# Optimization experiments

Hardware: AMD Instinct MI355X
Metric: run time of the kernel (lower is better)

Reference implementation:

```python
import jax, jax.numpy as jnp
import numpy as np

V, E, H, O, S, N = 32000, 256, 512, 32000, 128, 256

def setup_inputs() -> dict:
    key = jax.random.key(0)
    ks = jax.random.split(key, 12)
    s = 0.05
    return {
        'x': jax.random.randint(ks[0], (N, 1), 0, V),
        'encoder_outputs': jax.random.normal(ks[1], (N, S, 2 * H), jnp.float32),
        'hidden': jax.random.normal(ks[2], (1, N, H), jnp.float32),
        'cell': jax.random.normal(ks[3], (1, N, H), jnp.float32),
        'emb': jax.random.normal(ks[4], (V, E), jnp.float32) * s,
        'W_energy': jax.random.normal(ks[5], (1, 3 * H), jnp.float32) * s,
        'b_energy': jnp.zeros((1,), jnp.float32),
        'W_ih': jax.random.normal(ks[6], (4 * H, E + 2 * H), jnp.float32) * s,
        'W_hh': jax.random.normal(ks[7], (4 * H, H), jnp.float32) * s,
        'b_ih': jnp.zeros((4 * H,), jnp.float32),
        'b_hh': jnp.zeros((4 * H,), jnp.float32),
        'W_out': jax.random.normal(ks[8], (O, H), jnp.float32) * s,
        'b_out': jnp.zeros((O,), jnp.float32),
    }

def reference(x, encoder_outputs, hidden, cell, emb, W_energy, b_energy,
              W_ih, W_hh, b_ih, b_hh, W_out, b_out):
    # Dropout is identity at inference (eval mode).
    embedding = emb[x]                      # [N,1,E]
    n, s, _ = encoder_outputs.shape
    h = hidden[0]                            # [N,H] (num_layers==1)
    h_rep = jnp.broadcast_to(h[:, None, :], (n, s, h.shape[-1]))  # [N,S,H]
    feat = jnp.concatenate([h_rep, encoder_outputs], axis=-1)     # [N,S,3H]
    energy = jax.nn.relu(feat @ W_energy.T + b_energy)            # [N,S,1]
    attention = jax.nn.softmax(energy, axis=1)                    # softmax over seq
    context = jnp.einsum('nsk,nsl->nkl', attention, encoder_outputs)  # [N,1,2H]
    lstm_in = jnp.concatenate([context, embedding], axis=-1)[:, 0, :]  # [N,E+2H]
    gates = lstm_in @ W_ih.T + b_ih + h @ W_hh.T + b_hh           # [N,4H]
    i, f, g, o = jnp.split(gates, 4, axis=-1)                     # torch gate order
    i, f, o = jax.nn.sigmoid(i), jax.nn.sigmoid(f), jax.nn.sigmoid(o)
    g = jnp.tanh(g)
    c_new = f * cell[0] + i * g
    h_new = o * jnp.tanh(c_new)
    outputs = h_new[:, None, :]                                   # [N,1,H]
    predictions = outputs @ W_out.T + b_out                       # [N,1,O]
    return predictions, h_new[None], c_new[None]
```

## Files before the change

### kernel.cpp

```cpp
#include <hip/hip_runtime.h>
#include <hip/hip_bf16.h>

#define N_ 256
#define S_ 128
#define H_ 512
#define E_ 256
#define O_ 32000
#define KZ 1792
#define GJ 2048
#define KSPLIT 4
#define KCHUNK 448

typedef __attribute__((ext_vector_type(8))) short sv8;
typedef __attribute__((ext_vector_type(4))) float fv4;

__device__ __forceinline__ unsigned short f2bf(float f) {
  return __builtin_bit_cast(unsigned short, __float2bfloat16(f));
}

__device__ __forceinline__ sv8 pack8(fv4 a, fv4 b) {
  sv8 r;
  r[0] = (short)f2bf(a[0]); r[1] = (short)f2bf(a[1]);
  r[2] = (short)f2bf(a[2]); r[3] = (short)f2bf(a[3]);
  r[4] = (short)f2bf(b[0]); r[5] = (short)f2bf(b[1]);
  r[6] = (short)f2bf(b[2]); r[7] = (short)f2bf(b[3]);
  return r;
}

__global__ __launch_bounds__(1024) void k_attn(
    const int* __restrict__ x, const float* __restrict__ eo,
    const float* __restrict__ hid, const float* __restrict__ emb,
    const float* __restrict__ We, const float* __restrict__ be,
    const float* __restrict__ Wih, const float* __restrict__ Whh,
    unsigned short* __restrict__ Wgbf, unsigned short* __restrict__ z)
{
  if (blockIdx.y == 1) {
    const int tid = blockIdx.x * 1024 + threadIdx.x;
    for (int g = tid; g < 2048 * 224; g += 256 * 1024) {
      const int j = g / 224, c = g - j * 224;
      sv8* dst = (sv8*)(Wgbf + (size_t)j * KZ);
      if (c < 160) {
        const fv4* src = (const fv4*)(Wih + (size_t)j * 1280);
        dst[c] = pack8(src[2 * c], src[2 * c + 1]);
      } else {
        const int cc = c - 160;
        const fv4* src = (const fv4*)(Whh + (size_t)j * 512);
        dst[c] = pack8(src[2 * cc], src[2 * cc + 1]);
      }
    }
    return;
  }

  const int n = blockIdx.x;
  const int t = threadIdx.x;
  const int w = t >> 6;
  const int l = t & 63;

  __shared__ float s_red[16];
  __shared__ float s_m[16], s_l[16];
  __shared__ float s_ctx[16][1024];

  float hv = (t < 512) ? hid[(size_t)n * H_ + t] * We[t] : 0.f;
  #pragma unroll
  for (int off = 32; off >= 1; off >>= 1) hv += __shfl_xor(hv, off);
  if (l == 0) s_red[w] = hv;
  __syncthreads();
  float hWe = be[0];
  #pragma unroll
  for (int i = 0; i < 8; ++i) hWe += s_red[i];

  fv4 we0, we1, we2, we3;
  {
    const fv4* wp = (const fv4*)(We + H_);
    we0 = wp[l]; we1 = wp[l + 64]; we2 = wp[l + 128]; we3 = wp[l + 192];
  }

  float m = 0.f, lsum = 0.f;
  fv4 c0 = {0,0,0,0}, c1 = {0,0,0,0}, c2 = {0,0,0,0}, c3 = {0,0,0,0};
  const float* eob = eo + ((size_t)n * S_ + w * 8) * 1024;
  #pragma unroll 2
  for (int i = 0; i < 8; ++i) {
    const fv4* p = (const fv4*)(eob + (size_t)i * 1024);
    fv4 v0 = p[l], v1 = p[l + 64], v2 = p[l + 128], v3 = p[l + 192];
    float d = 0.f;
    #pragma unroll
    for (int c = 0; c < 4; ++c)
      d += v0[c]*we0[c] + v1[c]*we1[c] + v2[c]*we2[c] + v3[c]*we3[c];
    #pragma unroll
    for (int off = 32; off >= 1; off >>= 1) d += __shfl_xor(d, off);
    const float e  = fmaxf(d + hWe, 0.f);
    const float mn = fmaxf(m, e);
    const float sc = __expf(m - mn);
    const float pp = __expf(e - mn);
    lsum = lsum * sc + pp;
    #pragma unroll
    for (int c = 0; c < 4; ++c) {
      c0[c] = c0[c]*sc + pp*v0[c];
      c1[c] = c1[c]*sc + pp*v1[c];
      c2[c] = c2[c]*sc + pp*v2[c];
      c3[c] = c3[c]*sc + pp*v3[c];
    }
    m = mn;
  }
  if (l == 0) { s_m[w] = m; s_l[w] = lsum; }
  {
    fv4* sc_ = (fv4*)s_ctx[w];
    sc_[l] = c0; sc_[l+64] = c1; sc_[l+128] = c2; sc_[l+192] = c3;
  }
  __syncthreads();

  float M = s_m[0];
  #pragma unroll
  for (int i = 1; i < 16; ++i) M = fmaxf(M, s_m[i]);
  float wgt[16]; float L = 0.f;
  #pragma unroll
  for (int i = 0; i < 16; ++i) { wgt[i] = __expf(s_m[i] - M); L += wgt[i] * s_l[i]; }
  const float rL = 1.f / L;

  float acc = 0.f;
  #pragma unroll
  for (int i = 0; i < 16; ++i) acc += wgt[i] * s_ctx[i][t];
  unsigned short* zr = z + (size_t)n * KZ;
  zr[t] = f2bf(acc * rL);

  if (t < 256)       zr[1024 + t] = f2bf(emb[(size_t)x[n] * E_ + t]);
  else if (t < 768)  zr[1024 + t] = f2bf(hid[(size_t)n * H_ + (t - 256)]);
}

__global__ __launch_bounds__(256) void k_gates(
    const unsigned short* __restrict__ z, const unsigned short* __restrict__ Wgbf,
    float* __restrict__ part)
{
  const int j0 = blockIdx.x * 64;
  const int n0 = blockIdx.y * 64;
  const int kc = blockIdx.z * KCHUNK;
  const int t = threadIdx.x;
  const int w = t >> 6, l = t & 63;
  const int lr = l & 15, lg = l >> 4;
  const int jb = j0 + w * 16 + lr;

  const unsigned short* arow = z + kc + 8 * lg;
  const unsigned short* wrow = Wgbf + (size_t)jb * KZ + kc + 8 * lg;

  fv4 acc[4] = {{0,0,0,0},{0,0,0,0},{0,0,0,0},{0,0,0,0}};
  #pragma unroll
  for (int s = 0; s < 14; ++s) {
    const sv8 bf = *(const sv8*)(wrow + s * 32);
    #pragma unroll
    for (int f = 0; f < 4; ++f) {
      const sv8 af = *(const sv8*)(arow + (size_t)(n0 + f*16 + lr) * KZ + s * 32);
      acc[f] = __builtin_amdgcn_mfma_f32_16x16x32_bf16(af, bf, acc[f], 0, 0, 0);
    }
  }
  float* pp = part + (size_t)blockIdx.z * (N_ * GJ);
  #pragma unroll
  for (int f = 0; f < 4; ++f) {
    #pragma unroll
    for (int r = 0; r < 4; ++r)
      pp[(size_t)(n0 + f*16 + lg*4 + r) * GJ + jb] = acc[f][r];
  }
}

__global__ __launch_bounds__(256) void k_lstm(
    const float* __restrict__ part, const float* __restrict__ cell,
    const float* __restrict__ bih, const float* __restrict__ bhh,
    float* __restrict__ hout, float* __restrict__ cout,
    unsigned short* __restrict__ hbf)
{
  const int tid = blockIdx.x * 256 + threadIdx.x;
  const int n = tid >> 9, hh = tid & 511;
  const size_t base = (size_t)n * GJ;
  float ig = bih[hh]        + bhh[hh];
  float fg = bih[512 + hh]  + bhh[512 + hh];
  float gg = bih[1024 + hh] + bhh[1024 + hh];
  float og = bih[1536 + hh] + bhh[1536 + hh];
  #pragma unroll
  for (int k = 0; k < KSPLIT; ++k) {
    const float* p = part + (size_t)k * (N_ * GJ) + base;
    ig += p[hh];
    fg += p[512 + hh];
    gg += p[1024 + hh];
    og += p[1536 + hh];
  }
  ig = 1.f / (1.f + __expf(-ig));
  fg = 1.f / (1.f + __expf(-fg));
  og = 1.f / (1.f + __expf(-og));
  gg = tanhf(gg);
  const float c = fg * cell[tid] + ig * gg;
  const float h = og * tanhf(c);
  cout[tid] = c;
  hout[tid] = h;
  hbf[tid] = f2bf(h);
}

__global__ __launch_bounds__(512, 2) void k_pred(
    const unsigned short* __restrict__ hbf, const float* __restrict__ Wout,
    const float* __restrict__ bout, float* __restrict__ pred)
{
  __shared__ unsigned short Blds[64 * 512];
  const int o0 = blockIdx.x * 64;
  const int t = threadIdx.x;

  #pragma unroll
  for (int i = 0; i < 8; ++i) {
    const int g = t + i * 512;
    const int row = g >> 6, c = g & 63;
    const fv4* src = (const fv4*)(Wout + (size_t)(o0 + row) * H_ + c * 8);
    const sv8 v = pack8(src[0], src[1]);
    *(sv8*)((char*)Blds + row * 1024 + ((c * 16) ^ ((row & 7) << 4))) = v;
  }
  __syncthreads();

  const int w = t >> 6, l = t & 63;
  const int lr = l & 15, lg = l >> 4;
  const int nr = w * 32;

  fv4 acc[2][4] = {};
  #pragma unroll
  for (int kk = 0; kk < 16; ++kk) {
    sv8 a[2];
    #pragma unroll
    for (int f = 0; f < 2; ++f)
      a[f] = *(const sv8*)(hbf + (size_t)(nr + f*16 + lr) * H_ + kk*32 + 8*lg);
    #pragma unroll
    for (int fo = 0; fo < 4; ++fo) {
      const int row = fo * 16 + lr;
      const sv8 b = *(const sv8*)((const char*)Blds + row * 1024 +
                                  ((kk*64 + lg*16) ^ ((row & 7) << 4)));
      #pragma unroll
      for (int f = 0; f < 2; ++f)
        acc[f][fo] = __builtin_amdgcn_mfma_f32_16x16x32_bf16(b, a[f], acc[f][fo], 0, 0, 0);
    }
  }
  #pragma unroll
  for (int fo = 0; fo < 4; ++fo) {
    const int ob = o0 + fo * 16 + lg * 4;
    const fv4 bo4 = *(const fv4*)(bout + ob);
    #pragma unroll
    for (int f = 0; f < 2; ++f) {
      const int n = nr + f * 16 + lr;
      fv4 v;
      #pragma unroll
      for (int r = 0; r < 4; ++r) v[r] = acc[f][fo][r] + bo4[r];
      *(fv4*)(pred + (size_t)n * O_ + ob) = v;
    }
  }
}

extern "C" void kernel_launch(void* const* d_in, const int* in_sizes, int n_in,
                              void* d_out, int out_size, void* d_ws, size_t ws_size,
                              hipStream_t stream) {
  const int*   x    = (const int*)  d_in[0];
  const float* eo   = (const float*)d_in[1];
  const float* hid  = (const float*)d_in[2];
  const float* cell = (const float*)d_in[3];
  const float* emb  = (const float*)d_in[4];
  const float* We   = (const float*)d_in[5];
  const float* be   = (const float*)d_in[6];
  const float* Wih  = (const float*)d_in[7];
  const float* Whh  = (const float*)d_in[8];
  const float* bih  = (const float*)d_in[9];
  const float* bhh  = (const float*)d_in[10];
  const float* Wout = (const float*)d_in[11];
  const float* bout = (const float*)d_in[12];

  float* pred = (float*)d_out;
  float* hout = pred + (size_t)N_ * O_;
  float* cout = hout + (size_t)N_ * H_;

  unsigned short* z    = (unsigned short*)d_ws;
  unsigned short* hbf  = z + (size_t)N_ * KZ;
  float* part = (float*)(hbf + (size_t)N_ * H_);
  unsigned short* Wgbf = (unsigned short*)(part + (size_t)KSPLIT * N_ * GJ);

  k_attn <<<dim3(256, 2), 1024, 0, stream>>>(x, eo, hid, emb, We, be,
                                             Wih, Whh, Wgbf, z);
  k_gates<<<dim3(32, 4, KSPLIT), 256, 0, stream>>>(z, Wgbf, part);
  k_lstm <<<512, 256, 0, stream>>>(part, cell, bih, bhh, hout, cout, hbf);
  k_pred <<<500, 512, 0, stream>>>(hbf, Wout, bout, pred);
}
```

Baseline: 84.31 us.

## Fuse gates GEMM and LSTM cell into one kernel with grid barrier

Merges the split-K gate GEMM and the LSTM pointwise kernel into a single 512-block launch, separated by a software grid-wide barrier built on global atomics. The barrier counter is reset inside the attention kernel. This removes one kernel launch and its inter-kernel gap. In exchange it relies on all 512 blocks being co-resident, adds spin-wait overhead, and risks deadlock if the blocks cannot all be scheduled at once.

```diff
diff --git a/kernel.cpp b/kernel.cpp
--- a/kernel.cpp
+++ b/kernel.cpp
@@ -32,9 +32,11 @@
     const float* __restrict__ hid, const float* __restrict__ emb,
     const float* __restrict__ We, const float* __restrict__ be,
     const float* __restrict__ Wih, const float* __restrict__ Whh,
-    unsigned short* __restrict__ Wgbf, unsigned short* __restrict__ z)
+    unsigned short* __restrict__ Wgbf, unsigned short* __restrict__ z,
+    int* __restrict__ bar)
 {
   if (blockIdx.y == 1) {
+    if (blockIdx.x == 0 && threadIdx.x == 0) { bar[0] = 0; bar[1] = 0; }
     const int tid = blockIdx.x * 1024 + threadIdx.x;
     for (int g = tid; g < 2048 * 224; g += 256 * 1024) {
       const int j = g / 224, c = g - j * 224;
@@ -127,70 +129,89 @@
   else if (t < 768)  zr[1024 + t] = f2bf(hid[(size_t)n * H_ + (t - 256)]);
 }
 
-__global__ __launch_bounds__(256) void k_gates(
+__global__ __launch_bounds__(256) void k_gl(
     const unsigned short* __restrict__ z, const unsigned short* __restrict__ Wgbf,
-    float* __restrict__ part)
+    float* __restrict__ part, const float* __restrict__ cell,
+    const float* __restrict__ bih, const float* __restrict__ bhh,
+    float* __restrict__ hout, float* __restrict__ cout,
+    unsigned short* __restrict__ hbf, int* __restrict__ bar)
 {
-  const int j0 = blockIdx.x * 64;
-  const int n0 = blockIdx.y * 64;
-  const int kc = blockIdx.z * KCHUNK;
+  const int b = blockIdx.x;
   const int t = threadIdx.x;
   const int w = t >> 6, l = t & 63;
   const int lr = l & 15, lg = l >> 4;
-  const int jb = j0 + w * 16 + lr;
-
-  const unsigned short* arow = z + kc + 8 * lg;
-  const unsigned short* wrow = Wgbf + (size_t)jb * KZ + kc + 8 * lg;
-
-  fv4 acc[4] = {{0,0,0,0},{0,0,0,0},{0,0,0,0},{0,0,0,0}};
-  #pragma unroll
-  for (int s = 0; s < 14; ++s) {
-    const sv8 bf = *(const sv8*)(wrow + s * 32);
+
+  {
+    const int j0   = (b & 31) * 64;
+    const int n0   = ((b >> 5) & 3) * 64;
+    const int kidx = b >> 7;
+    const int kc   = kidx * KCHUNK;
+    const int jb   = j0 + w * 16 + lr;
+
+    const unsigned short* arow = z + kc + 8 * lg;
+    const unsigned short* wrow = Wgbf + (size_t)jb * KZ + kc + 8 * lg;
+
+    fv4 acc[4] = {{0,0,0,0},{0,0,0,0},{0,0,0,0},{0,0,0,0}};
+    #pragma unroll
+    for (int s = 0; s < 14; ++s) {
+      const sv8 bf = *(const sv8*)(wrow + s * 32);
+      #pragma unroll
+      for (int f = 0; f < 4; ++f) {
+        const sv8 af = *(const sv8*)(arow + (size_t)(n0 + f*16 + lr) * KZ + s * 32);
+        acc[f] = __builtin_amdgcn_mfma_f32_16x16x32_bf16(af, bf, acc[f], 0, 0, 0);
+      }
+    }
+    float* pp = part + (size_t)kidx * (N_ * GJ);
     #pragma unroll
     for (int f = 0; f < 4; ++f) {
-      const sv8 af = *(const sv8*)(arow + (size_t)(n0 + f*16 + lr) * KZ + s * 32);
-      acc[f] = __builtin_amdgcn_mfma_f32_16x16x32_bf16(af, bf, acc[f], 0, 0, 0);
-    }
-  }
-  float* pp = part + (size_t)blockIdx.z * (N_ * GJ);
-  #pragma unroll
-  for (int f = 0; f < 4; ++f) {
-    #pragma unroll
-    for (int r = 0; r < 4; ++r)
-      pp[(size_t)(n0 + f*16 + lg*4 + r) * GJ + jb] = acc[f][r];
-  }
-}
-
-__global__ __launch_bounds__(256) void k_lstm(
-    const float* __restrict__ part, const float* __restrict__ cell,
-    const float* __restrict__ bih, const float* __restrict__ bhh,
-    float* __restrict__ hout, float* __restrict__ cout,
-    unsigned short* __restrict__ hbf)
-{
-  const int tid = blockIdx.x * 256 + threadIdx.x;
-  const int n = tid >> 9, hh = tid & 511;
-  const size_t base = (size_t)n * GJ;
-  float ig = bih[hh]        + bhh[hh];
-  float fg = bih[512 + hh]  + bhh[512 + hh];
-  float gg = bih[1024 + hh] + bhh[1024 + hh];
-  float og = bih[1536 + hh] + bhh[1536 + hh];
-  #pragma unroll
-  for (int k = 0; k < KSPLIT; ++k) {
-    const float* p = part + (size_t)k * (N_ * GJ) + base;
-    ig += p[hh];
-    fg += p[512 + hh];
-    gg += p[1024 + hh];
-    og += p[1536 + hh];
-  }
-  ig = 1.f / (1.f + __expf(-ig));
-  fg = 1.f / (1.f + __expf(-fg));
-  og = 1.f / (1.f + __expf(-og));
-  gg = tanhf(gg);
-  const float c = fg * cell[tid] + ig * gg;
-  const float h = og * tanhf(c);
-  cout[tid] = c;
-  hout[tid] = h;
-  hbf[tid] = f2bf(h);
+      #pragma unroll
+      for (int r = 0; r < 4; ++r)
+        pp[(size_t)(n0 + f*16 + lg*4 + r) * GJ + jb] = acc[f][r];
+    }
+  }
+
+  __syncthreads();
+  __threadfence();
+  if (t == 0) {
+    const int g0 = __hip_atomic_load(&bar[1], __ATOMIC_ACQUIRE,
+                                     __HIP_MEMORY_SCOPE_AGENT);
+    if (atomicAdd(&bar[0], 1) == 511) {
+      __hip_atomic_store(&bar[0], 0, __ATOMIC_RELAXED, __HIP_MEMORY_SCOPE_AGENT);
+      __hip_atomic_store(&bar[1], g0 + 1, __ATOMIC_RELEASE,
+                         __HIP_MEMORY_SCOPE_AGENT);
+    } else {
+      while (__hip_atomic_load(&bar[1], __ATOMIC_ACQUIRE,
+                               __HIP_MEMORY_SCOPE_AGENT) == g0) {}
+    }
+  }
+  __syncthreads();
+
+  {
+    const int tid = b * 256 + t;
+    const int n = tid >> 9, hh = tid & 511;
+    const size_t base = (size_t)n * GJ;
+    float ig = bih[hh]        + bhh[hh];
+    float fg = bih[512 + hh]  + bhh[512 + hh];
+    float gg = bih[1024 + hh] + bhh[1024 + hh];
+    float og = bih[1536 + hh] + bhh[1536 + hh];
+    #pragma unroll
+    for (int k = 0; k < KSPLIT; ++k) {
+      const float* p = part + (size_t)k * (N_ * GJ) + base;
+      ig += p[hh];
+      fg += p[512 + hh];
+      gg += p[1024 + hh];
+      og += p[1536 + hh];
+    }
+    ig = 1.f / (1.f + __expf(-ig));
+    fg = 1.f / (1.f + __expf(-fg));
+    og = 1.f / (1.f + __expf(-og));
+    gg = tanhf(gg);
+    const float c = fg * cell[tid] + ig * gg;
+    const float h = og * tanhf(c);
+    cout[tid] = c;
+    hout[tid] = h;
+    hbf[tid] = f2bf(h);
+  }
 }
 
 __global__ __launch_bounds__(512, 2) void k_pred(
@@ -272,10 +293,11 @@
   unsigned short* hbf  = z + (size_t)N_ * KZ;
   float* part = (float*)(hbf + (size_t)N_ * H_);
   unsigned short* Wgbf = (unsigned short*)(part + (size_t)KSPLIT * N_ * GJ);
-
-  k_attn <<<dim3(256, 2), 1024, 0, stream>>>(x, eo, hid, emb, We, be,
-                                             Wih, Whh, Wgbf, z);
-  k_gates<<<dim3(32, 4, KSPLIT), 256, 0, stream>>>(z, Wgbf, part);
-  k_lstm <<<512, 256, 0, stream>>>(part, cell, bih, bhh, hout, cout, hbf);
-  k_pred <<<500, 512, 0, stream>>>(hbf, Wout, bout, pred);
-}
+  int* bar = (int*)(Wgbf + (size_t)GJ * KZ);
+
+  k_attn<<<dim3(256, 2), 1024, 0, stream>>>(x, eo, hid, emb, We, be,
+                                            Wih, Whh, Wgbf, z, bar);
+  k_gl  <<<512, 256, 0, stream>>>(z, Wgbf, part, cell, bih, bhh,
+                                  hout, cout, hbf, bar);
+  k_pred<<<500, 512, 0, stream>>>(hbf, Wout, bout, pred);
+}
```

New measurement: 182.7 us. 2.17x slower.
